# Kernel optimization log

Measured on AMD Instinct MI355X. Metric: run time of the kernel, lower is better.

Reference implementation:

```python
import jax, jax.numpy as jnp
import numpy as np

G_NUM, K_DEG = 3, 3  # grid intervals, spline order (module defaults)
LN_EPS = 1e-5


def _bspline_basis(x, grid, k):
    """Cox-de Boor B-spline basis. x: [N, D], grid: [D, G+2k+1] -> [N, D, G+k]."""
    xg = x[:, :, None]                      # [N, D, 1]
    g = grid[None, :, :]                    # [1, D, M]
    B = ((xg >= g[..., :-1]) & (xg < g[..., 1:])).astype(x.dtype)  # degree 0
    for d in range(1, k + 1):
        left = (xg - g[..., :-(d + 1)]) / (g[..., d:-1] - g[..., :-(d + 1)])
        right = (g[..., d + 1:] - xg) / (g[..., d + 1:] - g[..., 1:-d])
        B = left * B[..., :-1] + right * B[..., 1:]
    return B                                # [N, D, G+k]


def _kan_layer(x, grid, coef, scale_base, scale_sp, node_scale, node_bias):
    # spline branch: fold per-edge scale_sp into coef, contract basis without
    # materializing the [N, in, out] per-edge tensor
    basis = _bspline_basis(x, grid, K_DEG)              # [N, in, G+k]
    coef_eff = coef * scale_sp[..., None]               # [in, out, G+k]
    y = jnp.einsum('nib,iob->no', basis, coef_eff)      # spline sum over edges
    y = y + jax.nn.silu(x) @ scale_base                 # residual base function
    return node_scale * y + node_bias                   # per-node affine


def setup_inputs() -> dict:
    key = jax.random.key(0)
    ks = jax.random.split(key, 12)
    B, S = 16, 1024
    D0, D1, D2 = 256, 512, 256
    nb = G_NUM + K_DEG  # num basis fns = 6
    h = 2.0 / G_NUM
    knots = np.arange(-K_DEG, G_NUM + K_DEG + 1) * h - 1.0  # [G+2k+1]=10, range [-3,3]
    grid1 = jnp.asarray(np.tile(knots, (D0, 1)), jnp.float32)
    grid2 = jnp.asarray(np.tile(knots, (D1, 1)), jnp.float32)
    inp = {
        'x': jax.random.normal(ks[0], (B, S, D0), jnp.float32),
        'grid1': grid1,
        'coef1': jax.random.normal(ks[1], (D0, D1, nb), jnp.float32) * 0.1,
        'scale_base1': jax.random.normal(ks[2], (D0, D1), jnp.float32) / np.sqrt(D0),
        'scale_sp1': jnp.ones((D0, D1), jnp.float32),
        'node_scale1': jnp.ones((D1,), jnp.float32),
        'node_bias1': jnp.zeros((D1,), jnp.float32),
        'grid2': grid2,
        'coef2': jax.random.normal(ks[3], (D1, D2, nb), jnp.float32) * 0.1,
        'scale_base2': jax.random.normal(ks[4], (D1, D2), jnp.float32) / np.sqrt(D1),
        'scale_sp2': jnp.ones((D1, D2), jnp.float32),
        'node_scale2': jnp.ones((D2,), jnp.float32),
        'node_bias2': jnp.zeros((D2,), jnp.float32),
        'ln_gamma': jnp.ones((D2,), jnp.float32),
        'ln_beta': jnp.zeros((D2,), jnp.float32),
    }
    return inp


def reference(x, grid1, coef1, scale_base1, scale_sp1, node_scale1, node_bias1,
              grid2, coef2, scale_base2, scale_sp2, node_scale2, node_bias2,
              ln_gamma, ln_beta):
    b, s, d = x.shape
    residual = x  # start_dim == final_dim -> residual path active
    h = x.reshape(-1, d)
    h = _kan_layer(h, grid1, coef1, scale_base1, scale_sp1, node_scale1, node_bias1)
    h = _kan_layer(h, grid2, coef2, scale_base2, scale_sp2, node_scale2, node_bias2)
    h = h.reshape(b, s, -1)
    h = h + residual
    # LayerNorm over last dim
    mu = jnp.mean(h, axis=-1, keepdims=True)
    var = jnp.mean((h - mu) ** 2, axis=-1, keepdims=True)
    h = (h - mu) * jax.lax.rsqrt(var + LN_EPS) * ln_gamma + ln_beta
    # torch nn.GELU default is exact (erf) variant
    return jax.nn.gelu(h, approximate=False)
```

## Files before the change

kernel.cpp:

```cpp
#include <hip/hip_runtime.h>
#include <cstdint>
#include <cstddef>

using f16   = _Float16;
using half4 = __attribute__((ext_vector_type(4))) _Float16;
using half8 = __attribute__((ext_vector_type(8))) _Float16;
using f32x4 = __attribute__((ext_vector_type(4))) float;
using ull   = unsigned long long;

#define DINL __device__ __forceinline__

DINL void gload_lds16(const void* gptr, void* lptr) {
  __builtin_amdgcn_global_load_lds(
      reinterpret_cast<const __attribute__((address_space(1))) uint32_t*>(
          reinterpret_cast<uintptr_t>(gptr)),
      reinterpret_cast<__attribute__((address_space(3))) uint32_t*>(
          reinterpret_cast<uintptr_t>(lptr)),
      16, 0, 0);
}

DINL unsigned pkh(float a, float b) {
  unsigned short ha = __builtin_bit_cast(unsigned short, (f16)a);
  unsigned short hb = __builtin_bit_cast(unsigned short, (f16)b);
  return (unsigned)ha | ((unsigned)hb << 16);
}

struct U4 { unsigned x, y, z, w; };

DINL U4 expand_pack(float x) {
  float xs = (x + 3.0f) * 1.5f;
  float mf = floorf(xs);
  int   m  = (int)mf;
  float u = xs - mf, u2 = u * u, u3 = u2 * u, um = 1.0f - u;
  float p3 = u3 * (1.0f / 6.0f);
  float p2 = (1.0f + 3.0f * (u + u2 - u3)) * (1.0f / 6.0f);
  float p1 = (4.0f - 6.0f * u2 + 3.0f * u3) * (1.0f / 6.0f);
  float p0 = um * um * um * (1.0f / 6.0f);
  ull P = (ull)pkh(p0, p1) | ((ull)pkh(p2, p3) << 32);
  if ((unsigned)m > 8u) P = 0;
  int s    = m * 16 - 48;
  int sneg = min(63, max(0, -s));
  int spos = min(63, max(0, s));
  int shi2 = min(63, max(0, s - 64));
  ull rlo = (s < 0) ? (P >> sneg) : ((s < 64) ? (P << spos) : 0ull);
  ull rhi = (s < 0) ? 0ull
                    : ((s < 64) ? ((P >> (63 - spos)) >> 1) : (P << shi2));
  float sil = x / (1.0f + __expf(-x));
  U4 r;
  r.x = (unsigned)rlo;
  r.y = (unsigned)(rlo >> 32);
  r.z = (unsigned)rhi;
  r.w = pkh(sil, 0.0f);
  return r;
}

__global__ __launch_bounds__(256)
void prep_w_kernel(const float* __restrict__ coef, const float* __restrict__ ssp,
                   const float* __restrict__ sb, f16* __restrict__ Wt,
                   int Din, int Dout) {
  int idx = blockIdx.x * 256 + threadIdx.x;
  if (idx >= Din * Dout) return;
  int n = idx / Din;
  int d = idx - n * Din;
  float s = ssp[(size_t)d * Dout + n];
  const float* c = coef + ((size_t)d * Dout + n) * 6;
  half8 wv;
#pragma unroll
  for (int b = 0; b < 6; ++b) wv[b] = (f16)(c[b] * s);
  wv[6] = (f16)sb[(size_t)d * Dout + n];
  wv[7] = (f16)0.0f;
  int dp = (d & ~7) | ((d & 7) ^ (n & 7));
  *reinterpret_cast<half8*>(Wt + ((size_t)n * Din + dp) * 8) = wv;
}

template <bool BIAS, int NSRC, typename TIN, typename TOUT>
__global__ __launch_bounds__(256, 3)
void kan_gemm(const TIN* __restrict__ X0, const TIN* __restrict__ X1, int ldx,
              const f16* __restrict__ Wt, int ldw,
              const float* __restrict__ nscale, const float* __restrict__ nbias,
              int N, TOUT* __restrict__ Out, int nsteps) {
  __shared__ alignas(16) f16 AA[64 * 64];
  __shared__ alignas(16) f16 BB[256 * 64];

  const int tid  = threadIdx.x;
  const int w    = tid >> 6;
  const int lane = tid & 63;
  const int l15  = lane & 15, l7 = lane & 7, hi = lane >> 4;
  const int m0   = blockIdx.y * 64;
  const int n0   = blockIdx.x * 256;
  const int dim0 = blockIdx.z * (nsteps * 8);
  TOUT* outz = Out + (size_t)blockIdx.z * ((size_t)gridDim.y * 64) * N;

  const int ar = tid >> 3, ad = tid & 7;
  const TIN* a0 = X0 + (size_t)(m0 + ar) * ldx + dim0 + ad;
  const TIN* a1 = a0 + (size_t)32 * ldx;
  const TIN* b0 = nullptr;
  const TIN* b1 = nullptr;
  if constexpr (NSRC == 2) {
    b0 = X1 + (size_t)(m0 + ar) * ldx + dim0 + ad;
    b1 = b0 + (size_t)32 * ldx;
  }
  const int aoff0 = ar * 64 + 8 * (ad ^ (ar & 7));
  const int aoff1 = aoff0 + 32 * 64;

  auto loadx = [&](int doff, float& u, float& v) {
    u = (float)a0[doff];
    v = (float)a1[doff];
    if constexpr (NSRC == 2) {
      u += (float)b0[doff];
      v += (float)b1[doff];
    }
  };

  const f16* wsrc = Wt + (size_t)(n0 + (tid >> 3)) * ldw + (size_t)dim0 * 8 + (tid & 7) * 8;

  f32x4 acc[4][4] = {};

  auto stageB = [&](int k0) {
#pragma unroll
    for (int q = 0; q < 8; ++q)
      gload_lds16(wsrc + (size_t)q * 32 * ldw + k0, BB + tid * 8 + q * 2048);
  };

  auto compute = [&]() {
    __builtin_amdgcn_s_setprio(1);
#pragma unroll
    for (int kk = 0; kk < 2; ++kk) {
      const int sl = kk * 4 + hi;
      half8 av[4], bv[4];
#pragma unroll
      for (int i = 0; i < 4; ++i)
        av[i] = *reinterpret_cast<const half8*>(
            AA + (i * 16 + l15) * 64 + 8 * (sl ^ l7));
#pragma unroll
      for (int j = 0; j < 4; ++j)
        bv[j] = *reinterpret_cast<const half8*>(
            BB + (w * 64 + j * 16 + l15) * 64 + 8 * (sl ^ l7));
#pragma unroll
      for (int i = 0; i < 4; ++i)
#pragma unroll
        for (int j = 0; j < 4; ++j)
          acc[i][j] = __builtin_amdgcn_mfma_f32_16x16x32_f16(av[i], bv[j], acc[i][j], 0, 0, 0);
    }
    __builtin_amdgcn_s_setprio(0);
  };

  {
    float xu, xv;
    loadx(0, xu, xv);
    stageB(0);
    float yu0, yv0;
    loadx(8, yu0, yv0);
    U4 e0 = expand_pack(xu), e1 = expand_pack(xv);
    *reinterpret_cast<U4*>(AA + aoff0) = e0;
    *reinterpret_cast<U4*>(AA + aoff1) = e1;
    __syncthreads();

    float yu = yu0, yv = yv0;
    for (int s = 0; s < nsteps - 1; ++s) {
      compute();
      __syncthreads();
      stageB((s + 1) * 64);
      const int nd = (s + 2 < nsteps ? s + 2 : nsteps - 1) * 8;
      float zu, zv;
      loadx(nd, zu, zv);
      U4 e2 = expand_pack(yu), e3 = expand_pack(yv);
      *reinterpret_cast<U4*>(AA + aoff0) = e2;
      *reinterpret_cast<U4*>(AA + aoff1) = e3;
      yu = zu; yv = zv;
      __syncthreads();
    }
    compute();
  }

#pragma unroll
  for (int j = 0; j < 4; ++j) {
    int col   = n0 + w * 64 + j * 16 + l15;
    float nsv = nscale[col];
    float nbv = (BIAS && blockIdx.z == 0) ? nbias[col] : 0.0f;
#pragma unroll
    for (int i = 0; i < 4; ++i) {
      int rb = m0 + i * 16 + hi * 4;
#pragma unroll
      for (int r = 0; r < 4; ++r)
        outz[(size_t)(rb + r) * N + col] = (TOUT)(nsv * acc[i][j][r] + nbv);
    }
  }
}

__global__ __launch_bounds__(256)
void ln_gelu_kernel(const f16* __restrict__ P, size_t zstride,
                    const float* __restrict__ X,  const float* __restrict__ nb2,
                    const float* __restrict__ gamma, const float* __restrict__ beta,
                    float* __restrict__ out, int rows) {
  int row  = blockIdx.x * 4 + (threadIdx.x >> 6);
  int lane = threadIdx.x & 63;
  if (row >= rows) return;
  const size_t base = (size_t)row * 256 + lane * 4;
  const float4 xr = *reinterpret_cast<const float4*>(X + base);
  const float4 nb = *reinterpret_cast<const float4*>(nb2 + lane * 4);
  const float4 g  = *reinterpret_cast<const float4*>(gamma + lane * 4);
  const float4 be = *reinterpret_cast<const float4*>(beta + lane * 4);
  float h[4] = { (&nb.x)[0] + (&xr.x)[0], (&nb.x)[1] + (&xr.x)[1],
                 (&nb.x)[2] + (&xr.x)[2], (&nb.x)[3] + (&xr.x)[3] };
#pragma unroll
  for (int z = 0; z < 4; ++z) {
    const half4 p4 = *reinterpret_cast<const half4*>(P + z * zstride + base);
#pragma unroll
    for (int j = 0; j < 4; ++j) h[j] += (float)p4[j];
  }
  float s = h[0] + h[1] + h[2] + h[3];
#pragma unroll
  for (int o = 32; o >= 1; o >>= 1) s += __shfl_xor(s, o);
  float mu = s * (1.0f / 256.0f);
  float vs = 0.f;
#pragma unroll
  for (int j = 0; j < 4; ++j) { float d = h[j] - mu; vs += d * d; }
#pragma unroll
  for (int o = 32; o >= 1; o >>= 1) vs += __shfl_xor(vs, o);
  float inv = rsqrtf(vs * (1.0f / 256.0f) + 1e-5f);
  float o4[4];
#pragma unroll
  for (int j = 0; j < 4; ++j) {
    float v = (h[j] - mu) * inv * (&g.x)[j] + (&be.x)[j];
    o4[j] = 0.5f * v * (1.0f + erff(v * 0.70710678118654752f));
  }
  *reinterpret_cast<float4*>(out + (size_t)row * 256 + lane * 4) =
      make_float4(o4[0], o4[1], o4[2], o4[3]);
}

extern "C" void kernel_launch(void* const* d_in, const int* in_sizes, int n_in,
                              void* d_out, int out_size, void* d_ws, size_t ws_size,
                              hipStream_t stream) {
  (void)in_sizes; (void)n_in; (void)out_size; (void)ws_size;
  const float* x     = (const float*)d_in[0];
  const float* coef1 = (const float*)d_in[2];
  const float* sb1   = (const float*)d_in[3];
  const float* ssp1  = (const float*)d_in[4];
  const float* ns1   = (const float*)d_in[5];
  const float* nb1   = (const float*)d_in[6];
  const float* coef2 = (const float*)d_in[8];
  const float* sb2   = (const float*)d_in[9];
  const float* ssp2  = (const float*)d_in[10];
  const float* ns2   = (const float*)d_in[11];
  const float* nb2   = (const float*)d_in[12];
  const float* lgam  = (const float*)d_in[13];
  const float* lbet  = (const float*)d_in[14];
  float* out = (float*)d_out;

  const int Ntok = 16 * 1024;
  const int D0 = 256, D1 = 512, D2 = 256;

  char* ws     = (char*)d_ws;
  f16*  h1p    = (f16*)ws;
  size_t h1z   = (size_t)Ntok * D1;
  size_t off   = 2 * h1z * sizeof(f16);
  f16*  part   = (f16*)(ws + off);
  size_t partz = (size_t)Ntok * D2;
  off += 4 * partz * sizeof(f16);
  f16* Wt1 = (f16*)(ws + off);
  off += (size_t)D1 * D0 * 8 * sizeof(f16);
  f16* Wt2 = (f16*)(ws + off);

  prep_w_kernel<<<(D0 * D1 + 255) / 256, 256, 0, stream>>>(coef1, ssp1, sb1, Wt1, D0, D1);
  prep_w_kernel<<<(D1 * D2 + 255) / 256, 256, 0, stream>>>(coef2, ssp2, sb2, Wt2, D1, D2);

  kan_gemm<true, 1, float, f16><<<dim3(D1 / 256, Ntok / 64, 2), 256, 0, stream>>>(
      x, nullptr, D0, Wt1, D0 * 8, ns1, nb1, D1, h1p, D0 / 16);

  kan_gemm<false, 2, f16, f16><<<dim3(D2 / 256, Ntok / 64, 4), 256, 0, stream>>>(
      h1p, h1p + h1z, D1, Wt2, D1 * 8, ns2, nullptr, D2, part, D1 / 32);

  ln_gelu_kernel<<<Ntok / 4, 256, 0, stream>>>(
      part, partz, x, nb2, lgam, lbet, out, Ntok);
}
```

Baseline: 131.1 us.

## Rewrite KAN GEMM as 256x256 double-buffered 8-wave kernel with async X staging

```diff
diff --git a/kernel.cpp b/kernel.cpp
--- a/kernel.cpp
+++ b/kernel.cpp
@@ -55,11 +55,22 @@
 }
 
 __global__ __launch_bounds__(256)
-void prep_w_kernel(const float* __restrict__ coef, const float* __restrict__ ssp,
-                   const float* __restrict__ sb, f16* __restrict__ Wt,
-                   int Din, int Dout) {
+void prep_w2_kernel(const float* __restrict__ coef1, const float* __restrict__ ssp1,
+                    const float* __restrict__ sb1,   f16* __restrict__ Wt1, int n1,
+                    const float* __restrict__ coef2, const float* __restrict__ ssp2,
+                    const float* __restrict__ sb2,   f16* __restrict__ Wt2,
+                    int Din1, int Dout1, int Din2, int Dout2) {
   int idx = blockIdx.x * 256 + threadIdx.x;
-  if (idx >= Din * Dout) return;
+  const float *coef, *ssp, *sb;
+  f16* Wt;
+  int Din, Dout;
+  if (idx < n1) {
+    coef = coef1; ssp = ssp1; sb = sb1; Wt = Wt1; Din = Din1; Dout = Dout1;
+  } else {
+    idx -= n1;
+    if (idx >= Din2 * Dout2) return;
+    coef = coef2; ssp = ssp2; sb = sb2; Wt = Wt2; Din = Din2; Dout = Dout2;
+  }
   int n = idx / Din;
   int d = idx - n * Din;
   float s = ssp[(size_t)d * Dout + n];
@@ -74,113 +85,196 @@
 }
 
 template <bool BIAS, int NSRC, typename TIN, typename TOUT>
-__global__ __launch_bounds__(256, 3)
-void kan_gemm(const TIN* __restrict__ X0, const TIN* __restrict__ X1, int ldx,
-              const f16* __restrict__ Wt, int ldw,
-              const float* __restrict__ nscale, const float* __restrict__ nbias,
-              int N, TOUT* __restrict__ Out, int nsteps) {
-  __shared__ alignas(16) f16 AA[64 * 64];
-  __shared__ alignas(16) f16 BB[256 * 64];
+__global__ __launch_bounds__(512, 1)
+void kan_gemm8(const TIN* __restrict__ X0, const TIN* __restrict__ X1, int ldx,
+               const f16* __restrict__ Wt, int ldw,
+               const float* __restrict__ nscale, const float* __restrict__ nbias,
+               int N, TOUT* __restrict__ Out, int T) {
+  extern __shared__ char smem[];
+  f16*  A0v = (f16*)(smem);
+  f16*  A1v = (f16*)(smem + 32768);
+  f16*  B0v = (f16*)(smem + 65536);
+  f16*  B1v = (f16*)(smem + 98304);
+  char* Xb0 = smem + 131072;
+  char* Xb1 = smem + 131072 + 8192;
 
   const int tid  = threadIdx.x;
+  const int lane = tid & 63;
   const int w    = tid >> 6;
-  const int lane = tid & 63;
   const int l15  = lane & 15, l7 = lane & 7, hi = lane >> 4;
-  const int m0   = blockIdx.y * 64;
+  const int wm   = w >> 2, wn = w & 3;
+  const int m0   = blockIdx.y * 256;
   const int n0   = blockIdx.x * 256;
-  const int dim0 = blockIdx.z * (nsteps * 8);
-  TOUT* outz = Out + (size_t)blockIdx.z * ((size_t)gridDim.y * 64) * N;
-
-  const int ar = tid >> 3, ad = tid & 7;
-  const TIN* a0 = X0 + (size_t)(m0 + ar) * ldx + dim0 + ad;
-  const TIN* a1 = a0 + (size_t)32 * ldx;
-  const TIN* b0 = nullptr;
-  const TIN* b1 = nullptr;
-  if constexpr (NSRC == 2) {
-    b0 = X1 + (size_t)(m0 + ar) * ldx + dim0 + ad;
-    b1 = b0 + (size_t)32 * ldx;
-  }
-  const int aoff0 = ar * 64 + 8 * (ad ^ (ar & 7));
-  const int aoff1 = aoff0 + 32 * 64;
-
-  auto loadx = [&](int doff, float& u, float& v) {
-    u = (float)a0[doff];
-    v = (float)a1[doff];
-    if constexpr (NSRC == 2) {
-      u += (float)b0[doff];
-      v += (float)b1[doff];
-    }
+  const int dim0 = blockIdx.z * (T * 8);
+  TOUT* outz = Out + (size_t)blockIdx.z * ((size_t)gridDim.y * 256) * N;
+
+  const f16* wb[4];
+  int bdst[4];
+#pragma unroll
+  for (int q = 0; q < 4; ++q) {
+    int c   = tid + q * 512;
+    wb[q]   = Wt + (size_t)(n0 + (c >> 3)) * ldw + (size_t)dim0 * 8 + (c & 7) * 8;
+    bdst[q] = c * 8;
+  }
+
+  const int er = tid >> 1, ed0 = 4 * (tid & 1), erq = er & 7;
+  const TIN* xsrc;
+  if constexpr (NSRC == 1) {
+    xsrc = X0 + (size_t)(m0 + er) * ldx + dim0 + ed0;
+  } else {
+    xsrc = (tid < 256) ? (X0 + (size_t)(m0 + tid) * ldx + dim0)
+                       : (X1 + (size_t)(m0 + tid - 256) * ldx + dim0);
+  }
+
+  const int aRow = (wm * 128 + l15) * 64;
+  const int bRow = (wn * 64 + l15) * 64;
+  const int s0 = 8 * (hi ^ l7);
+  const int s1 = 8 * ((4 + hi) ^ l7);
+
+  f32x4 acc[8][4] = {};
+
+  auto stageB2 = [&](f16* Bn, int kB, int qb) {
+    gload_lds16(wb[qb] + kB, Bn + bdst[qb]);
+    gload_lds16(wb[qb + 1] + kB, Bn + bdst[qb + 1]);
   };
-
-  const f16* wsrc = Wt + (size_t)(n0 + (tid >> 3)) * ldw + (size_t)dim0 * 8 + (tid & 7) * 8;
-
-  f32x4 acc[4][4] = {};
-
-  auto stageB = [&](int k0) {
-#pragma unroll
-    for (int q = 0; q < 8; ++q)
-      gload_lds16(wsrc + (size_t)q * 32 * ldw + k0, BB + tid * 8 + q * 2048);
+  auto stageX = [&](char* Xw, int dX) {
+    gload_lds16(xsrc + dX, Xw + tid * 16);
   };
-
-  auto compute = [&]() {
+  auto loadx = [&](const char* Xr, float* xs) {
+    if constexpr (NSRC == 1) {
+      const float4 v = *reinterpret_cast<const float4*>(
+          (const float*)Xr + er * 8 + ed0);
+      xs[0] = v.x; xs[1] = v.y; xs[2] = v.z; xs[3] = v.w;
+    } else {
+      const f16* p = (const f16*)Xr;
+      half4 a = *reinterpret_cast<const half4*>(p + er * 8 + ed0);
+      half4 b = *reinterpret_cast<const half4*>(p + 2048 + er * 8 + ed0);
+#pragma unroll
+      for (int j = 0; j < 4; ++j) xs[j] = (float)a[j] + (float)b[j];
+    }
+  };
+
+  auto TILE = [&](const f16* Ac, const f16* Bc, f16* An, f16* Bn,
+                  const char* Xr, char* Xw, int kB, int dX) {
+    half8 av[4], bv[4];
+#pragma unroll
+    for (int i = 0; i < 4; ++i)
+      av[i] = *reinterpret_cast<const half8*>(Ac + aRow + i * 1024 + s0);
+#pragma unroll
+    for (int j = 0; j < 4; ++j)
+      bv[j] = *reinterpret_cast<const half8*>(Bc + bRow + j * 1024 + s0);
+    stageB2(Bn, kB, 0);
+    __builtin_amdgcn_s_barrier();
     __builtin_amdgcn_s_setprio(1);
 #pragma unroll
-    for (int kk = 0; kk < 2; ++kk) {
-      const int sl = kk * 4 + hi;
-      half8 av[4], bv[4];
-#pragma unroll
-      for (int i = 0; i < 4; ++i)
-        av[i] = *reinterpret_cast<const half8*>(
-            AA + (i * 16 + l15) * 64 + 8 * (sl ^ l7));
+    for (int i = 0; i < 4; ++i)
 #pragma unroll
       for (int j = 0; j < 4; ++j)
-        bv[j] = *reinterpret_cast<const half8*>(
-            BB + (w * 64 + j * 16 + l15) * 64 + 8 * (sl ^ l7));
-#pragma unroll
-      for (int i = 0; i < 4; ++i)
-#pragma unroll
-        for (int j = 0; j < 4; ++j)
-          acc[i][j] = __builtin_amdgcn_mfma_f32_16x16x32_f16(av[i], bv[j], acc[i][j], 0, 0, 0);
-    }
+        acc[i][j] = __builtin_amdgcn_mfma_f32_16x16x32_f16(av[i], bv[j], acc[i][j], 0, 0, 0);
     __builtin_amdgcn_s_setprio(0);
+    __builtin_amdgcn_s_barrier();
+#pragma unroll
+    for (int i = 0; i < 4; ++i)
+      av[i] = *reinterpret_cast<const half8*>(Ac + aRow + (4 + i) * 1024 + s0);
+    stageB2(Bn, kB, 2);
+    __builtin_amdgcn_s_barrier();
+    __builtin_amdgcn_s_setprio(1);
+#pragma unroll
+    for (int i = 0; i < 4; ++i)
+#pragma unroll
+      for (int j = 0; j < 4; ++j)
+        acc[4 + i][j] = __builtin_amdgcn_mfma_f32_16x16x32_f16(av[i], bv[j], acc[4 + i][j], 0, 0, 0);
+    __builtin_amdgcn_s_setprio(0);
+    asm volatile("s_waitcnt vmcnt(4)" ::: "memory");
+    __builtin_amdgcn_sched_barrier(0);
+    __builtin_amdgcn_s_barrier();
+#pragma unroll
+    for (int i = 0; i < 4; ++i)
+      av[i] = *reinterpret_cast<const half8*>(Ac + aRow + i * 1024 + s1);
+#pragma unroll
+    for (int j = 0; j < 4; ++j)
+      bv[j] = *reinterpret_cast<const half8*>(Bc + bRow + j * 1024 + s1);
+    float xs[4];
+    loadx(Xr, xs);
+    stageX(Xw, dX);
+    {
+      U4 e0 = expand_pack(xs[0]);
+      U4 e1 = expand_pack(xs[1]);
+      *reinterpret_cast<U4*>(An + er * 64 + 8 * ((ed0 + 0) ^ erq)) = e0;
+      *reinterpret_cast<U4*>(An + er * 64 + 8 * ((ed0 + 1) ^ erq)) = e1;
+    }
+    __builtin_amdgcn_s_barrier();
+    __builtin_amdgcn_s_setprio(1);
+#pragma unroll
+    for (int i = 0; i < 4; ++i)
+#pragma unroll
+      for (int j = 0; j < 4; ++j)
+        acc[i][j] = __builtin_amdgcn_mfma_f32_16x16x32_f16(av[i], bv[j], acc[i][j], 0, 0, 0);
+    __builtin_amdgcn_s_setprio(0);
+    __builtin_amdgcn_s_barrier();
+#pragma unroll
+    for (int i = 0; i < 4; ++i)
+      av[i] = *reinterpret_cast<const half8*>(Ac + aRow + (4 + i) * 1024 + s1);
+    {
+      U4 e2 = expand_pack(xs[2]);
+      U4 e3 = expand_pack(xs[3]);
+      *reinterpret_cast<U4*>(An + er * 64 + 8 * ((ed0 + 2) ^ erq)) = e2;
+      *reinterpret_cast<U4*>(An + er * 64 + 8 * ((ed0 + 3) ^ erq)) = e3;
+    }
+    __builtin_amdgcn_s_barrier();
+    __builtin_amdgcn_s_setprio(1);
+#pragma unroll
+    for (int i = 0; i < 4; ++i)
+#pragma unroll
+      for (int j = 0; j < 4; ++j)
+        acc[4 + i][j] = __builtin_amdgcn_mfma_f32_16x16x32_f16(av[i], bv[j], acc[4 + i][j], 0, 0, 0);
+    __builtin_amdgcn_s_setprio(0);
+    asm volatile("s_waitcnt lgkmcnt(0)" ::: "memory");
+    asm volatile("s_waitcnt vmcnt(1)" ::: "memory");
+    __builtin_amdgcn_sched_barrier(0);
+    __builtin_amdgcn_s_barrier();
   };
 
+  stageX(Xb0, 0);
+  stageB2(B0v, 0, 0);
+  stageB2(B0v, 0, 2);
+  stageX(Xb1, (T > 1 ? 8 : 0));
+  asm volatile("s_waitcnt vmcnt(5)" ::: "memory");
+  __builtin_amdgcn_sched_barrier(0);
+  __builtin_amdgcn_s_barrier();
   {
-    float xu, xv;
-    loadx(0, xu, xv);
-    stageB(0);
-    float yu0, yv0;
-    loadx(8, yu0, yv0);
-    U4 e0 = expand_pack(xu), e1 = expand_pack(xv);
-    *reinterpret_cast<U4*>(AA + aoff0) = e0;
-    *reinterpret_cast<U4*>(AA + aoff1) = e1;
-    __syncthreads();
-
-    float yu = yu0, yv = yv0;
-    for (int s = 0; s < nsteps - 1; ++s) {
-      compute();
-      __syncthreads();
-      stageB((s + 1) * 64);
-      const int nd = (s + 2 < nsteps ? s + 2 : nsteps - 1) * 8;
-      float zu, zv;
-      loadx(nd, zu, zv);
-      U4 e2 = expand_pack(yu), e3 = expand_pack(yv);
-      *reinterpret_cast<U4*>(AA + aoff0) = e2;
-      *reinterpret_cast<U4*>(AA + aoff1) = e3;
-      yu = zu; yv = zv;
-      __syncthreads();
-    }
-    compute();
+    float xs[4];
+    loadx(Xb0, xs);
+#pragma unroll
+    for (int j = 0; j < 4; ++j) {
+      U4 e = expand_pack(xs[j]);
+      *reinterpret_cast<U4*>(A0v + er * 64 + 8 * ((ed0 + j) ^ erq)) = e;
+    }
+  }
+  asm volatile("s_waitcnt lgkmcnt(0)" ::: "memory");
+  asm volatile("s_waitcnt vmcnt(1)" ::: "memory");
+  __builtin_amdgcn_sched_barrier(0);
+  __builtin_amdgcn_s_barrier();
+
+  const int npairs = T >> 1;
+  for (int p = 0; p < npairs; ++p) {
+    const int t0 = 2 * p, t1 = 2 * p + 1;
+    const int kB0 = (t0 + 1 < T ? t0 + 1 : T - 1) * 64;
+    const int dX0 = (t0 + 2 < T ? t0 + 2 : T - 1) * 8;
+    const int kB1 = (t1 + 1 < T ? t1 + 1 : T - 1) * 64;
+    const int dX1 = (t1 + 2 < T ? t1 + 2 : T - 1) * 8;
+    TILE(A0v, B0v, A1v, B1v, Xb1, Xb0, kB0, dX0);
+    TILE(A1v, B1v, A0v, B0v, Xb0, Xb1, kB1, dX1);
   }
 
 #pragma unroll
   for (int j = 0; j < 4; ++j) {
-    int col   = n0 + w * 64 + j * 16 + l15;
+    int col   = n0 + wn * 64 + j * 16 + l15;
     float nsv = nscale[col];
     float nbv = (BIAS && blockIdx.z == 0) ? nbias[col] : 0.0f;
 #pragma unroll
-    for (int i = 0; i < 4; ++i) {
-      int rb = m0 + i * 16 + hi * 4;
+    for (int i = 0; i < 8; ++i) {
+      int rb = m0 + wm * 128 + i * 16 + hi * 4;
 #pragma unroll
       for (int r = 0; r < 4; ++r)
         outz[(size_t)(rb + r) * N + col] = (TOUT)(nsv * acc[i][j][r] + nbv);
@@ -250,6 +344,7 @@
 
   const int Ntok = 16 * 1024;
   const int D0 = 256, D1 = 512, D2 = 256;
+  const size_t LDS = 147456;
 
   char* ws     = (char*)d_ws;
   f16*  h1p    = (f16*)ws;
@@ -262,13 +357,14 @@
   off += (size_t)D1 * D0 * 8 * sizeof(f16);
   f16* Wt2 = (f16*)(ws + off);
 
-  prep_w_kernel<<<(D0 * D1 + 255) / 256, 256, 0, stream>>>(coef1, ssp1, sb1, Wt1, D0, D1);
-  prep_w_kernel<<<(D1 * D2 + 255) / 256, 256, 0, stream>>>(coef2, ssp2, sb2, Wt2, D1, D2);
-
-  kan_gemm<true, 1, float, f16><<<dim3(D1 / 256, Ntok / 64, 2), 256, 0, stream>>>(
+  const int n1 = D0 * D1, n2 = D1 * D2;
+  prep_w2_kernel<<<(n1 + n2 + 255) / 256, 256, 0, stream>>>(
+      coef1, ssp1, sb1, Wt1, n1, coef2, ssp2, sb2, Wt2, D0, D1, D1, D2);
+
+  kan_gemm8<true, 1, float, f16><<<dim3(D1 / 256, Ntok / 256, 2), 512, LDS, stream>>>(
       x, nullptr, D0, Wt1, D0 * 8, ns1, nb1, D1, h1p, D0 / 16);
 
-  kan_gemm<false, 2, f16, f16><<<dim3(D2 / 256, Ntok / 64, 4), 256, 0, stream>>>(
+  kan_gemm8<false, 2, f16, f16><<<dim3(D2 / 256, Ntok / 256, 4), 512, LDS, stream>>>(
       h1p, h1p + h1z, D1, Wt2, D1 * 8, ns2, nullptr, D2, part, D1 / 32);
 
   ln_gelu_kernel<<<Ntok / 4, 256, 0, stream>>>(
```

Result: slower. 140.9 us (+7.5%).
